# Optimization experiments

Measured on AMD Instinct MI355X. Metric: run time of the kernel, lower is better.

The kernel has to match this reference:

```python
import jax, jax.numpy as jnp
import numpy as np
from itertools import combinations

S = 7                       # number of species (H,C,N,O,S,F,Cl)
RCR, RCA = 5.2, 3.5         # radial / angular cutoffs (Angstrom)
ETA_R, ETA_A, ZETA = 19.7, 12.5, 14.1
SHF_R = jnp.asarray(0.8 + 0.275 * np.arange(16), jnp.float32)        # 16 radial shifts
SHF_A = jnp.asarray(0.8 + 0.3375 * np.arange(8), jnp.float32)        # 8 angular radial shifts
SHF_Z = jnp.asarray((np.arange(4) + 0.5) * np.pi / 4, jnp.float32)   # 4 angle shifts
NPAIR = S * (S + 1) // 2    # 28 unordered species pairs
_t = np.zeros((S, S), np.int32); _c = 0
for _a in range(S):
    for _b in range(_a, S):
        _t[_a, _b] = _t[_b, _a] = _c; _c += 1
TRIU = jnp.asarray(_t)
AEV_DIM = S * 16 + NPAIR * 32   # 1008
M, H1, H2, H3 = 8, 256, 192, 160  # ensemble size and MLP widths


def _fc(d, rc):
    # torchani cutoff_cosine, masked for safety beyond rc
    return jnp.where(d < rc, 0.5 * jnp.cos(jnp.pi * d / rc) + 0.5, 0.0)


def compute_aev(sp, coords, atom_index12, triplet_index):
    # sp:[N] int, coords:[N,3], atom_index12:[2,P] half neighbor list,
    # triplet_index:[3,T] = (center, neighbor_j, neighbor_k)
    N = sp.shape[0]
    i, j = atom_index12[0], atom_index12[1]
    dvec = coords[j] - coords[i]
    dist = jnp.sqrt((dvec * dvec).sum(-1))
    fc = _fc(dist, RCR)
    rterm = 0.25 * jnp.exp(-ETA_R * (dist[:, None] - SHF_R) ** 2) * fc[:, None]  # [P,16]
    rad = jnp.zeros((N * S, 16), rterm.dtype)
    rad = rad.at[i * S + sp[j]].add(rterm).at[j * S + sp[i]].add(rterm)
    rad = rad.reshape(N, S * 16)

    c, a, b = triplet_index[0], triplet_index[1], triplet_index[2]
    v1 = coords[a] - coords[c]
    v2 = coords[b] - coords[c]
    d1 = jnp.sqrt((v1 * v1).sum(-1))
    d2 = jnp.sqrt((v2 * v2).sum(-1))
    cosang = 0.95 * (v1 * v2).sum(-1) / (d1 * d2)   # 0.95 numerical-safety factor as in torchani
    ang = jnp.arccos(cosang)
    fcj = _fc(d1, RCA) * _fc(d2, RCA)
    f1 = ((1.0 + jnp.cos(ang[:, None] - SHF_Z)) / 2.0) ** ZETA              # [T,4]
    f2 = jnp.exp(-ETA_A * ((d1 + d2)[:, None] / 2.0 - SHF_A) ** 2)          # [T,8]
    aterm = 2.0 * (f2[:, :, None] * f1[:, None, :]).reshape(-1, 32) * fcj[:, None]  # [T,32]
    pidx = TRIU[sp[a], sp[b]]
    angv = jnp.zeros((N * NPAIR, 32), aterm.dtype).at[c * NPAIR + pidx].add(aterm)
    return jnp.concatenate([rad, angv.reshape(N, NPAIR * 32)], axis=-1)     # [N,1008]


def _energy_and_force(species, coordinates, atom_index12, triplet_index, sgp,
                      W1, b1, W2, b2, W3, b3, W4, b4, sae):
    sp = species[0]
    sgpv = sgp[0]

    def total(coords):
        aev = compute_aev(sp, coords[0], atom_index12, triplet_index)       # [N,1008]
        h = jax.nn.celu(jnp.einsum('na,msab->msnb', aev, W1) + b1[:, :, None, :], alpha=0.1)
        h = jax.nn.celu(jnp.einsum('msnb,msbc->msnc', h, W2) + b2[:, :, None, :], alpha=0.1)
        h = jax.nn.celu(jnp.einsum('msnc,mscd->msnd', h, W3) + b3[:, :, None, :], alpha=0.1)
        e = jnp.einsum('msnd,msd->msn', h, W4) + b4[:, :, None]             # [M,S,N]
        onehot = (sgpv[None, :] == jnp.arange(S)[:, None]).astype(e.dtype)  # ghosts (-1) -> all-zero
        atomic = (e * onehot[None]).sum(1).mean(0)                           # [N] ensemble mean
        atomic = atomic + jnp.where(sgpv >= 0, sae[jnp.clip(sgpv, 0)], 0.0)  # energy shifter SAEs
        return atomic.sum()

    E = total(coordinates)
    force = -jax.grad(total)(coordinates)   # autograd force as in forward_total
    return E[None], force


def setup_inputs() -> dict:
    key = jax.random.key(0)
    n = 14; N = n ** 3   # 2744 atoms on a jittered cubic lattice (2.5 A spacing)
    ar = np.arange(n)
    gx, gy, gz = np.meshgrid(ar, ar, ar, indexing='ij')
    pos = np.stack([gx, gy, gz], -1).reshape(-1, 3)
    lid = lambda p: (p[:, 0] * n + p[:, 1]) * n + p[:, 2]
    # half neighbor list: all lattice offsets with |r| <= 5.2/2.5 lattice units
    half = [(1,0,0),(0,1,0),(0,0,1),(1,1,0),(1,-1,0),(1,0,1),(1,0,-1),(0,1,1),(0,1,-1),
            (1,1,1),(1,1,-1),(1,-1,1),(1,-1,-1),(2,0,0),(0,2,0),(0,0,2)]
    ei, ej = [], []
    for off in half:
        q = pos + np.array(off)
        m = ((q >= 0) & (q < n)).all(1)
        ei.append(lid(pos[m])); ej.append(lid(q[m]))
    atom_index12 = np.stack([np.concatenate(ei), np.concatenate(ej)]).astype(np.int32)
    # angular triplets: pairs of unit-offset neighbors (within Rca=3.5 A) per center
    unit = [(1,0,0),(-1,0,0),(0,1,0),(0,-1,0),(0,0,1),(0,0,-1)]
    nb = np.full((N, 6), -1, np.int64)
    for t, off in enumerate(unit):
        q = pos + np.array(off)
        m = ((q >= 0) & (q < n)).all(1)
        nb[lid(pos[m]), t] = lid(q[m])
    tc, tj, tk = [], [], []
    for a_, b_ in combinations(range(6), 2):
        m = (nb[:, a_] >= 0) & (nb[:, b_] >= 0)
        tc.append(np.nonzero(m)[0]); tj.append(nb[m, a_]); tk.append(nb[m, b_])
    triplet_index = np.stack([np.concatenate(tc), np.concatenate(tj), np.concatenate(tk)]).astype(np.int32)
    rng = np.random.default_rng(0)
    species = rng.integers(0, S, (1, N)).astype(np.int32)
    nghost = 250
    sgp = species.copy(); sgp[0, N - nghost:] = -1   # ghost atoms padded with -1
    coords = (pos.astype(np.float32) * 2.5 + 0.15 * rng.standard_normal((N, 3)).astype(np.float32))[None]
    ks = jax.random.split(key, 9)
    D = AEV_DIM
    W1 = jax.random.normal(ks[0], (M, S, D, H1), jnp.float32) * (D ** -0.5)
    b1 = 0.01 * jax.random.normal(ks[1], (M, S, H1), jnp.float32)
    W2 = jax.random.normal(ks[2], (M, S, H1, H2), jnp.float32) * (H1 ** -0.5)
    b2 = 0.01 * jax.random.normal(ks[3], (M, S, H2), jnp.float32)
    W3 = jax.random.normal(ks[4], (M, S, H2, H3), jnp.float32) * (H2 ** -0.5)
    b3 = 0.01 * jax.random.normal(ks[5], (M, S, H3), jnp.float32)
    W4 = jax.random.normal(ks[6], (M, S, H3), jnp.float32) * (H3 ** -0.5)
    b4 = 0.01 * jax.random.normal(ks[7], (M, S), jnp.float32)
    sae = jax.random.normal(ks[8], (S,), jnp.float32)
    return {
        'species': jnp.asarray(species), 'coordinates': jnp.asarray(coords),
        'atom_index12': jnp.asarray(atom_index12), 'triplet_index': jnp.asarray(triplet_index),
        'species_ghost_as_padding': jnp.asarray(sgp),
        'W1': W1, 'b1': b1, 'W2': W2, 'b2': b2, 'W3': W3, 'b3': b3, 'W4': W4, 'b4': b4, 'sae': sae,
    }


def reference(species, coordinates, atom_index12, triplet_index, species_ghost_as_padding,
              W1, b1, W2, b2, W3, b3, W4, b4, sae):
    return _energy_and_force(species, coordinates, atom_index12, triplet_index,
                             species_ghost_as_padding, W1, b1, W2, b2, W3, b3, W4, b4, sae)
```

## Files before the change

kernel.cpp:

```cpp
#include <hip/hip_runtime.h>
#include <math.h>

constexpr int SPEC = 7;
constexpr int DAEV = 1008;
constexpr int RADN = 112;
constexpr int H1W = 256, H2W = 192, H3W = 160;
constexpr int MENS = 8;
constexpr float ALPHA = 0.1f;
constexpr float RCR_ = 5.2f, RCA_ = 3.5f;
constexpr float ETAR = 19.7f, ETAA = 12.5f, ZETA_ = 14.1f;
constexpr float PIF = 3.14159265358979323846f;

enum { MODE_FWD = 0, MODE_BWD = 1, MODE_PLAIN = 2 };

typedef _Float16 f16x8 __attribute__((ext_vector_type(8)));
typedef float f32x4 __attribute__((ext_vector_type(4)));

__device__ __forceinline__ f32x4 mfma16(f16x8 a, f16x8 b, f32x4 c) {
    return __builtin_amdgcn_mfma_f32_16x16x32_f16(a, b, c, 0, 0, 0);
}

__device__ __forceinline__ void cvt8(float4 u0, float4 u1, f16x8& h, f16x8& l) {
    float x[8] = {u0.x, u0.y, u0.z, u0.w, u1.x, u1.y, u1.z, u1.w};
    #pragma unroll
    for (int e = 0; e < 8; ++e) {
        _Float16 hh = (_Float16)x[e];
        h[e] = hh;
        l[e] = (_Float16)(x[e] - (float)hh);
    }
}

__global__ __launch_bounds__(256) void build_lists_k(
    const int* __restrict__ sgp, int* __restrict__ counts,
    int* __restrict__ lists, int N)
{
    int n = blockIdx.x * blockDim.x + threadIdx.x;
    if (n >= N) return;
    int g = sgp[n];
    if (g >= 0) {
        int p = atomicAdd(&counts[g], 1);
        lists[g * N + p] = n;
    }
}

__global__ __launch_bounds__(256) void radial_fwd_k(
    const int* __restrict__ ai12, const int* __restrict__ spec,
    const float* __restrict__ coord, float* __restrict__ aev, int P)
{
    int p = blockIdx.x * blockDim.x + threadIdx.x;
    if (p >= P) return;
    int i = ai12[p], j = ai12[P + p];
    float dx = coord[3 * j + 0] - coord[3 * i + 0];
    float dy = coord[3 * j + 1] - coord[3 * i + 1];
    float dz = coord[3 * j + 2] - coord[3 * i + 2];
    float d = sqrtf(dx * dx + dy * dy + dz * dz);
    float fc = (d < RCR_) ? (0.5f * cosf(PIF * d / RCR_) + 0.5f) : 0.f;
    int spi = spec[i], spj = spec[j];
    float* bi = aev + (size_t)i * DAEV + spj * 16;
    float* bj = aev + (size_t)j * DAEV + spi * 16;
    #pragma unroll
    for (int k = 0; k < 16; ++k) {
        float sh = 0.8f + 0.275f * k;
        float t = d - sh;
        float v = 0.25f * expf(-ETAR * t * t) * fc;
        atomicAdd(bi + k, v);
        atomicAdd(bj + k, v);
    }
}

__global__ __launch_bounds__(256) void angular_fwd_k(
    const int* __restrict__ tri, const int* __restrict__ spec,
    const float* __restrict__ coord, float* __restrict__ aev, int T)
{
    int t = blockIdx.x * blockDim.x + threadIdx.x;
    if (t >= T) return;
    int c = tri[t], a = tri[T + t], b = tri[2 * T + t];
    float cx = coord[3 * c], cy = coord[3 * c + 1], cz = coord[3 * c + 2];
    float v1x = coord[3 * a] - cx, v1y = coord[3 * a + 1] - cy, v1z = coord[3 * a + 2] - cz;
    float v2x = coord[3 * b] - cx, v2y = coord[3 * b + 1] - cy, v2z = coord[3 * b + 2] - cz;
    float d1 = sqrtf(v1x * v1x + v1y * v1y + v1z * v1z);
    float d2 = sqrtf(v2x * v2x + v2y * v2y + v2z * v2z);
    float u = v1x * v2x + v1y * v2y + v1z * v2z;
    float ca = 0.95f * u / (d1 * d2);
    float sa = sqrtf(fmaxf(1.f - ca * ca, 0.f));
    float fc1 = (d1 < RCA_) ? (0.5f * cosf(PIF * d1 / RCA_) + 0.5f) : 0.f;
    float fc2 = (d2 < RCA_) ? (0.5f * cosf(PIF * d2 / RCA_) + 0.5f) : 0.f;
    float fcj = fc1 * fc2;
    float savg = 0.5f * (d1 + d2);
    int s1 = spec[a], s2 = spec[b];
    int lo = min(s1, s2), hi = max(s1, s2);
    int pidx = lo * SPEC - (lo * (lo - 1)) / 2 + (hi - lo);
    float* ob = aev + (size_t)c * DAEV + RADN + pidx * 32;
    const float CZ[4] = {0.92387953f, 0.38268343f, -0.38268343f, -0.92387953f};
    const float SZ[4] = {0.38268343f, 0.92387953f, 0.92387953f, 0.38268343f};
    float f1[4];
    #pragma unroll
    for (int zz = 0; zz < 4; ++zz) {
        float cd = ca * CZ[zz] + sa * SZ[zz];
        float base = fmaxf(0.5f * (1.f + cd), 0.f);
        f1[zz] = powf(base, ZETA_);
    }
    #pragma unroll
    for (int q = 0; q < 8; ++q) {
        float sh = 0.8f + 0.3375f * q;
        float tq = savg - sh;
        float f2 = expf(-ETAA * tq * tq);
        float b2 = 2.f * f2 * fcj;
        #pragma unroll
        for (int zz = 0; zz < 4; ++zz)
            atomicAdd(ob + q * 4 + zz, b2 * f1[zz]);
    }
}

template<bool DO_O, bool DO_T>
__global__ __launch_bounds__(256) void wconv_k(
    const float* __restrict__ W,
    _Float16* __restrict__ oH, _Float16* __restrict__ oL,
    _Float16* __restrict__ tH, _Float16* __restrict__ tL,
    int K, int C, int ldt)
{
    __shared__ _Float16 sh[64][65];
    __shared__ _Float16 sl[64][65];
    const int z = blockIdx.z;
    const int k0 = blockIdx.y * 64, c0 = blockIdx.x * 64;
    const float* Wz = W + (size_t)z * K * C;
    const int c = threadIdx.x & 63, qr = threadIdx.x >> 6;
    #pragma unroll
    for (int rr = 0; rr < 16; ++rr) {
        int r = qr * 16 + rr;
        int k = k0 + r, cc = c0 + c;
        float v = (k < K && cc < C) ? Wz[(size_t)k * C + cc] : 0.f;
        _Float16 h = (_Float16)v;
        _Float16 l = (_Float16)(v - (float)h);
        if (DO_O && k < K && cc < C) {
            oH[(size_t)z * K * C + (size_t)k * C + cc] = h;
            oL[(size_t)z * K * C + (size_t)k * C + cc] = l;
        }
        if (DO_T) { sh[r][c] = h; sl[r][c] = l; }
    }
    if (DO_T) {
        __syncthreads();
        #pragma unroll
        for (int rr = 0; rr < 16; ++rr) {
            int r = qr * 16 + rr;
            int crow = c0 + r, kcol = k0 + c;
            if (crow < C && kcol < ldt) {
                tH[(size_t)z * C * ldt + (size_t)crow * ldt + kcol] = sh[c][r];
                tL[(size_t)z * C * ldt + (size_t)crow * ldt + kcol] = sl[c][r];
            }
        }
    }
}

template<int MODE, int ASRC, int BSRC, bool MCONCAT, int SPLITK>
__global__ __launch_bounds__(512) void mgemm_k(
    const void* __restrict__ Ah_, const void* __restrict__ Al_,
    const void* __restrict__ Bh_, const void* __restrict__ Bl_,
    const float* __restrict__ bias, float* __restrict__ cF,
    _Float16* __restrict__ cH, _Float16* __restrict__ cL,
    const int* __restrict__ lists, const int* __restrict__ counts,
    int N, int K, int KA, int H, int lda, int ldb, int ldc,
    size_t aStrM, size_t bStrZ, size_t cStrM)
{
    __shared__ f16x8 SM[3072];
    __shared__ int atomsS[64];
    #define AhS(g, kq, i) SM[(g) * 256 + (kq) * 64 + (i)]
    #define AlS(g, kq, i) SM[512 + (g) * 256 + (kq) * 64 + (i)]
    #define BhS(g, kq, c) SM[1024 + (g) * 512 + (kq) * 128 + (c)]
    #define BlS(g, kq, c) SM[2048 + (g) * 512 + (kq) * 128 + (c)]

    int bx = blockIdx.x, by = blockIdx.y, bz = blockIdx.z;
    if (gridDim.z == 56) {
        int BXY = gridDim.x * gridDim.y;
        int flat = bx + gridDim.x * (by + gridDim.y * bz);
        int xcd = flat & 7;
        int rest = flat >> 3;
        int zw = rest / BXY;
        int xy = rest - zw * BXY;
        bz = xcd * 7 + zw;
        bx = xy % gridDim.x;
        by = xy / gridDim.x;
    }

    const int z = bz;
    int m, sp_, chunk;
    if (MCONCAT) {
        sp_ = (SPLITK > 1) ? (z % SPEC) : z;
        chunk = (SPLITK > 1) ? (z / SPEC) : 0;
        m = 0;
    } else {
        m = z / SPEC; sp_ = z - m * SPEC; chunk = 0;
    }
    const int cnt = counts[sp_];
    const int row0 = by * 64;
    if (row0 >= cnt) return;
    const int col0 = bx * 128;
    const int tid = threadIdx.x;
    const int w = tid >> 6, lane = tid & 63;
    const int g = w >> 2, wl = w & 3;

    const int rA = min(row0 + lane, cnt - 1);
    const int atomA = lists[sp_ * N + rA];
    if (tid < 64) atomsS[tid] = atomA;

    const int bc0 = min(col0 + lane, H - 1);
    const int bc1 = min(col0 + 64 + lane, H - 1);

    f16x8 rAh, rAl;
    float4 rAf0, rAf1;
    f16x8 rBh0, rBl0, rBh1, rBl1;
    float4 rBq[4];
    float rB0f[8], rB1f[8];

    auto LOAD = [&](int k0s) {
        int kk = k0s + wl * 8;
        if constexpr (ASRC == 0) {
            const _Float16* ah = (const _Float16*)Ah_;
            const _Float16* al = (const _Float16*)Al_;
            size_t ao;
            if constexpr (MCONCAT) {
                int mm = kk >> 8, kr = kk & 255;
                ao = ((size_t)mm * N + atomA) * (size_t)lda + kr;
            } else {
                ao = (size_t)m * aStrM + (size_t)atomA * lda + kk;
            }
            rAh = *(const f16x8*)(ah + ao);
            rAl = *(const f16x8*)(al + ao);
        } else {
            const float* af = (const float*)Ah_;
            if (kk < KA) {
                const float* p = af + (size_t)atomA * lda + kk;
                rAf0 = *(const float4*)p;
                rAf1 = *(const float4*)(p + 4);
            } else {
                rAf0 = make_float4(0.f, 0.f, 0.f, 0.f);
                rAf1 = rAf0;
            }
        }
        if constexpr (BSRC == 0) {
            const _Float16* bh = (const _Float16*)Bh_;
            const _Float16* bl = (const _Float16*)Bl_;
            size_t b0 = (size_t)z * bStrZ + (size_t)bc0 * ldb + kk;
            size_t b1 = (size_t)z * bStrZ + (size_t)bc1 * ldb + kk;
            rBh0 = *(const f16x8*)(bh + b0);
            rBh1 = *(const f16x8*)(bh + b1);
            rBl0 = *(const f16x8*)(bl + b0);
            rBl1 = *(const f16x8*)(bl + b1);
        } else if constexpr (BSRC == 1) {
            const float* bf = (const float*)Bh_;
            int mm = kk >> 8, kr = kk & 255;
            size_t b0 = ((size_t)(mm * SPEC + sp_) * DAEV + bc0) * (size_t)ldb + kr;
            size_t b1 = ((size_t)(mm * SPEC + sp_) * DAEV + bc1) * (size_t)ldb + kr;
            rBq[0] = *(const float4*)(bf + b0);
            rBq[1] = *(const float4*)(bf + b0 + 4);
            rBq[2] = *(const float4*)(bf + b1);
            rBq[3] = *(const float4*)(bf + b1 + 4);
        } else {
            const float* bf = (const float*)Bh_ + (size_t)z * bStrZ;
            #pragma unroll
            for (int j = 0; j < 8; ++j) {
                int kg = kk + j;
                float v0 = 0.f, v1 = 0.f;
                if (kg < KA) {
                    v0 = bf[(size_t)kg * ldb + bc0];
                    v1 = bf[(size_t)kg * ldb + bc1];
                }
                rB0f[j] = v0;
                rB1f[j] = v1;
            }
        }
    };

    auto WRITE = [&]() {
        if constexpr (ASRC == 0) {
            AhS(g, wl, lane) = rAh;
            AlS(g, wl, lane) = rAl;
        } else {
            f16x8 h, l;
            cvt8(rAf0, rAf1, h, l);
            AhS(g, wl, lane) = h;
            AlS(g, wl, lane) = l;
        }
        if constexpr (BSRC == 0) {
            BhS(g, wl, lane) = rBh0;
            BhS(g, wl, 64 + lane) = rBh1;
            BlS(g, wl, lane) = rBl0;
            BlS(g, wl, 64 + lane) = rBl1;
        } else if constexpr (BSRC == 1) {
            f16x8 h, l;
            cvt8(rBq[0], rBq[1], h, l);
            BhS(g, wl, lane) = h;
            BlS(g, wl, lane) = l;
            cvt8(rBq[2], rBq[3], h, l);
            BhS(g, wl, 64 + lane) = h;
            BlS(g, wl, 64 + lane) = l;
        } else {
            f16x8 h0, l0, h1, l1;
            #pragma unroll
            for (int j = 0; j < 8; ++j) {
                _Float16 ha = (_Float16)rB0f[j];
                h0[j] = ha; l0[j] = (_Float16)(rB0f[j] - (float)ha);
                _Float16 hb = (_Float16)rB1f[j];
                h1[j] = hb; l1[j] = (_Float16)(rB1f[j] - (float)hb);
            }
            BhS(g, wl, lane) = h0;
            BlS(g, wl, lane) = l0;
            BhS(g, wl, 64 + lane) = h1;
            BlS(g, wl, 64 + lane) = l1;
        }
    };

    const int wr = wl >> 1, wc = wl & 1;
    const int fr = lane & 15, q = lane >> 4;

    f32x4 acc[2][4];
    #pragma unroll
    for (int mi = 0; mi < 2; ++mi)
        #pragma unroll
        for (int ni = 0; ni < 4; ++ni)
            acc[mi][ni] = (f32x4){0.f, 0.f, 0.f, 0.f};

    const int KC = (SPLITK > 1) ? (K / SPLITK) : K;
    const int kbeg = chunk * KC;
    const int ntT = KC / 32;
    const int nt0 = (ntT + 1) >> 1;
    const int my_nt = g ? (ntT - nt0) : nt0;
    const int gk = kbeg + (g ? nt0 * 32 : 0);

    if (my_nt > 0) LOAD(gk);

    for (int t = 0; t < nt0; ++t) {
        __syncthreads();
        if (t < my_nt) WRITE();
        __syncthreads();
        if (t + 1 < my_nt) LOAD(gk + (t + 1) * 32);

        if (t < my_nt) {
            f16x8 fah[2], fal[2], fbh[4], fbl[4];
            #pragma unroll
            for (int mi = 0; mi < 2; ++mi) {
                int r = wr * 32 + mi * 16 + fr;
                fah[mi] = AhS(g, q, r);
                fal[mi] = AlS(g, q, r);
            }
            #pragma unroll
            for (int ni = 0; ni < 4; ++ni) {
                int c = wc * 64 + ni * 16 + fr;
                fbh[ni] = BhS(g, q, c);
                fbl[ni] = BlS(g, q, c);
            }
            #pragma unroll
            for (int mi = 0; mi < 2; ++mi)
                #pragma unroll
                for (int ni = 0; ni < 4; ++ni) {
                    acc[mi][ni] = mfma16(fah[mi], fbl[ni], acc[mi][ni]);
                    acc[mi][ni] = mfma16(fal[mi], fbh[ni], acc[mi][ni]);
                    acc[mi][ni] = mfma16(fah[mi], fbh[ni], acc[mi][ni]);
                }
        }
    }

    __syncthreads();
    f32x4* X = (f32x4*)SM;
    const int xbase = (wl * 64 + lane) * 8;
    if (g == 1) {
        #pragma unroll
        for (int mi = 0; mi < 2; ++mi)
            #pragma unroll
            for (int ni = 0; ni < 4; ++ni)
                X[xbase + mi * 4 + ni] = acc[mi][ni];
    }
    __syncthreads();
    if (g == 1) return;
    #pragma unroll
    for (int mi = 0; mi < 2; ++mi)
        #pragma unroll
        for (int ni = 0; ni < 4; ++ni) {
            f32x4 o = X[xbase + mi * 4 + ni];
            acc[mi][ni] += o;
        }

    const float* brow = (MODE == MODE_FWD) ? (bias + (size_t)z * H) : nullptr;
    #pragma unroll
    for (int mi = 0; mi < 2; ++mi) {
        #pragma unroll
        for (int r = 0; r < 4; ++r) {
            int rl = wr * 32 + mi * 16 + q * 4 + r;
            if (row0 + rl >= cnt) continue;
            int atom = atomsS[rl];
            size_t rowoff = (size_t)m * cStrM + (size_t)atom * ldc;
            #pragma unroll
            for (int ni = 0; ni < 4; ++ni) {
                int col = col0 + wc * 64 + ni * 16 + fr;
                if (col >= H) continue;
                float v = acc[mi][ni][r];
                size_t idx = rowoff + col;
                if (MODE == MODE_FWD) {
                    v += brow[col];
                    v = (v > 0.f) ? v : ALPHA * expm1f(v * (1.f / ALPHA));
                    _Float16 hh = (_Float16)v;
                    cH[idx] = hh;
                    cL[idx] = (_Float16)(v - (float)hh);
                } else if (MODE == MODE_BWD) {
                    float hprev = (float)cH[idx] + (float)cL[idx];
                    float D = (hprev > 0.f) ? 1.f : (hprev * (1.f / ALPHA) + 1.f);
                    v *= D;
                    _Float16 hh = (_Float16)v;
                    cH[idx] = hh;
                    cL[idx] = (_Float16)(v - (float)hh);
                } else {
                    if (SPLITK > 1) atomicAdd(cF + idx, v);
                    else cF[idx] = v;
                }
            }
        }
    }
    #undef AhS
    #undef AlS
    #undef BhS
    #undef BlS
}

__global__ __launch_bounds__(256) void l4_k(
    _Float16* __restrict__ h3H, _Float16* __restrict__ h3L,
    const float* __restrict__ W4, const float* __restrict__ b4,
    const int* __restrict__ lists, const int* __restrict__ counts,
    float* __restrict__ Eout, int N)
{
    const int z = blockIdx.y;
    const int m = z / SPEC, s = z - m * SPEC;
    const int cnt = counts[s];
    const int sub = threadIdx.x >> 3;
    const int l8 = threadIdx.x & 7;
    const int row = blockIdx.x * 32 + sub;

    __shared__ float bsum;
    if (threadIdx.x == 0) bsum = 0.f;
    __syncthreads();

    if (row < cnt) {
        int atom = lists[s * N + row];
        size_t base = ((size_t)m * N + atom) * H3W;
        const float* w4 = W4 + (size_t)z * H3W;
        float sum = 0.f;
        for (int k = l8; k < H3W; k += 8) {
            float h = (float)h3H[base + k] + (float)h3L[base + k];
            float wv = w4[k];
            sum += h * wv;
            float D = (h > 0.f) ? 1.f : (h * 10.f + 1.f);
            float g = 0.125f * wv * D;
            _Float16 gh = (_Float16)g;
            h3H[base + k] = gh;
            h3L[base + k] = (_Float16)(g - (float)gh);
        }
        sum += __shfl_xor(sum, 1);
        sum += __shfl_xor(sum, 2);
        sum += __shfl_xor(sum, 4);
        if (l8 == 0) atomicAdd(&bsum, sum + b4[z]);
    }
    __syncthreads();
    if (threadIdx.x == 0) atomicAdd(Eout, 0.125f * bsum);
}

__global__ __launch_bounds__(256) void radial_bwd_k(
    const int* __restrict__ ai12, const int* __restrict__ spec,
    const float* __restrict__ coord, const float* __restrict__ daev,
    float* __restrict__ grad, int P)
{
    int p = blockIdx.x * blockDim.x + threadIdx.x;
    if (p >= P) return;
    int i = ai12[p], j = ai12[P + p];
    float dx = coord[3 * j + 0] - coord[3 * i + 0];
    float dy = coord[3 * j + 1] - coord[3 * i + 1];
    float dz = coord[3 * j + 2] - coord[3 * i + 2];
    float d = sqrtf(dx * dx + dy * dy + dz * dz);
    float fc, dfc;
    if (d < RCR_) {
        float ph = PIF * d / RCR_;
        fc = 0.5f * cosf(ph) + 0.5f;
        dfc = -0.5f * sinf(ph) * (PIF / RCR_);
    } else { fc = 0.f; dfc = 0.f; }
    int spi = spec[i], spj = spec[j];
    const float* gi = daev + (size_t)i * DAEV + spj * 16;
    const float* gj = daev + (size_t)j * DAEV + spi * 16;
    float gs = 0.f;
    #pragma unroll
    for (int k = 0; k < 16; ++k) {
        float sh = 0.8f + 0.275f * k;
        float t = d - sh;
        float ex = expf(-ETAR * t * t);
        float g = gi[k] + gj[k];
        gs += g * 0.25f * ex * (dfc - 2.f * ETAR * t * fc);
    }
    float invd = 1.f / d;
    float gx = gs * dx * invd, gy = gs * dy * invd, gz = gs * dz * invd;
    atomicAdd(&grad[3 * j + 0], gx);  atomicAdd(&grad[3 * j + 1], gy);  atomicAdd(&grad[3 * j + 2], gz);
    atomicAdd(&grad[3 * i + 0], -gx); atomicAdd(&grad[3 * i + 1], -gy); atomicAdd(&grad[3 * i + 2], -gz);
}

__global__ __launch_bounds__(256) void angular_bwd_k(
    const int* __restrict__ tri, const int* __restrict__ spec,
    const float* __restrict__ coord, const float* __restrict__ daev,
    float* __restrict__ grad, int T)
{
    int t = blockIdx.x * blockDim.x + threadIdx.x;
    if (t >= T) return;
    int c = tri[t], a = tri[T + t], b = tri[2 * T + t];
    float cx = coord[3 * c], cy = coord[3 * c + 1], cz = coord[3 * c + 2];
    float v1x = coord[3 * a] - cx, v1y = coord[3 * a + 1] - cy, v1z = coord[3 * a + 2] - cz;
    float v2x = coord[3 * b] - cx, v2y = coord[3 * b + 1] - cy, v2z = coord[3 * b + 2] - cz;
    float d1 = sqrtf(v1x * v1x + v1y * v1y + v1z * v1z);
    float d2 = sqrtf(v2x * v2x + v2y * v2y + v2z * v2z);
    float u = v1x * v2x + v1y * v2y + v1z * v2z;
    float inv12 = 1.f / (d1 * d2);
    float ca = 0.95f * u * inv12;
    float sa = sqrtf(fmaxf(1.f - ca * ca, 1e-12f));
    float fc1, dfc1, fc2, dfc2;
    if (d1 < RCA_) {
        float ph = PIF * d1 / RCA_;
        fc1 = 0.5f * cosf(ph) + 0.5f;
        dfc1 = -0.5f * sinf(ph) * (PIF / RCA_);
    } else { fc1 = 0.f; dfc1 = 0.f; }
    if (d2 < RCA_) {
        float ph = PIF * d2 / RCA_;
        fc2 = 0.5f * cosf(ph) + 0.5f;
        dfc2 = -0.5f * sinf(ph) * (PIF / RCA_);
    } else { fc2 = 0.f; dfc2 = 0.f; }
    float fcj = fc1 * fc2;
    float savg = 0.5f * (d1 + d2);
    int s1 = spec[a], s2 = spec[b];
    int lo = min(s1, s2), hi = max(s1, s2);
    int pidx = lo * SPEC - (lo * (lo - 1)) / 2 + (hi - lo);
    const float* gb = daev + (size_t)c * DAEV + RADN + pidx * 32;
    const float CZ[4] = {0.92387953f, 0.38268343f, -0.38268343f, -0.92387953f};
    const float SZ[4] = {0.38268343f, 0.92387953f, 0.92387953f, 0.38268343f};
    float f1[4], df1[4];
    #pragma unroll
    for (int zz = 0; zz < 4; ++zz) {
        float cd = ca * CZ[zz] + sa * SZ[zz];
        float sd = sa * CZ[zz] - ca * SZ[zz];
        float base = fmaxf(0.5f * (1.f + cd), 0.f);
        float pm1 = powf(base, ZETA_ - 1.f);
        f1[zz] = pm1 * base;
        df1[zz] = ZETA_ * pm1 * (-0.5f * sd);
    }
    float A_ = 0.f, B_ = 0.f, Cc = 0.f;
    #pragma unroll
    for (int q = 0; q < 8; ++q) {
        float sh = 0.8f + 0.3375f * q;
        float tq = savg - sh;
        float f2 = expf(-ETAA * tq * tq);
        float df2 = -ETAA * tq * f2;
        #pragma unroll
        for (int zz = 0; zz < 4; ++zz) {
            float G2 = 2.f * gb[q * 4 + zz];
            A_ += G2 * f2 * df1[zz];
            B_ += G2 * df2 * f1[zz];
            Cc += G2 * f2 * f1[zz];
        }
    }
    A_ *= fcj; B_ *= fcj;
    float C1 = Cc * dfc1 * fc2;
    float C2 = Cc * fc1 * dfc2;
    float cA = -A_ / sa;
    float k12 = cA * 0.95f * inv12;
    float coef1 = (cA * (-ca) / d1 + B_ + C1) / d1;
    float coef2 = (cA * (-ca) / d2 + B_ + C2) / d2;
    float g1x = coef1 * v1x + k12 * v2x;
    float g1y = coef1 * v1y + k12 * v2y;
    float g1z = coef1 * v1z + k12 * v2z;
    float g2x = coef2 * v2x + k12 * v1x;
    float g2y = coef2 * v2y + k12 * v1y;
    float g2z = coef2 * v2z + k12 * v1z;
    atomicAdd(&grad[3 * a + 0], g1x); atomicAdd(&grad[3 * a + 1], g1y); atomicAdd(&grad[3 * a + 2], g1z);
    atomicAdd(&grad[3 * b + 0], g2x); atomicAdd(&grad[3 * b + 1], g2y); atomicAdd(&grad[3 * b + 2], g2z);
    atomicAdd(&grad[3 * c + 0], -(g1x + g2x));
    atomicAdd(&grad[3 * c + 1], -(g1y + g2y));
    atomicAdd(&grad[3 * c + 2], -(g1z + g2z));
}

__global__ __launch_bounds__(256) void finalize_k(
    const float* __restrict__ grad, const int* __restrict__ sgp,
    const float* __restrict__ sae, float* __restrict__ out, int N)
{
    int n = blockIdx.x * blockDim.x + threadIdx.x;
    __shared__ float bs;
    if (threadIdx.x == 0) bs = 0.f;
    __syncthreads();
    float v = 0.f;
    if (n < N) {
        out[1 + 3 * n + 0] = -grad[3 * n + 0];
        out[1 + 3 * n + 1] = -grad[3 * n + 1];
        out[1 + 3 * n + 2] = -grad[3 * n + 2];
        int g = sgp[n];
        if (g >= 0) v = sae[g];
    }
    atomicAdd(&bs, v);
    __syncthreads();
    if (threadIdx.x == 0) atomicAdd(out, bs);
}

extern "C" void kernel_launch(void* const* d_in, const int* in_sizes, int n_in,
                              void* d_out, int out_size, void* d_ws, size_t ws_size,
                              hipStream_t stream)
{
    (void)n_in; (void)out_size; (void)ws_size;
    const int* species = (const int*)d_in[0];
    const float* coords = (const float*)d_in[1];
    const int* ai12 = (const int*)d_in[2];
    const int* tri = (const int*)d_in[3];
    const int* sgp = (const int*)d_in[4];
    const float* W1 = (const float*)d_in[5];
    const float* b1 = (const float*)d_in[6];
    const float* W2 = (const float*)d_in[7];
    const float* b2 = (const float*)d_in[8];
    const float* W3 = (const float*)d_in[9];
    const float* b3 = (const float*)d_in[10];
    const float* W4 = (const float*)d_in[11];
    const float* b4 = (const float*)d_in[12];
    const float* sae = (const float*)d_in[13];
    float* out = (float*)d_out;

    const int N = in_sizes[0];
    const int P = in_sizes[2] / 2;
    const int T = in_sizes[3] / 3;
    const size_t NM = (size_t)MENS * N;

    float* ws = (float*)d_ws;
    size_t off = 0;
    auto alloc = [&](size_t nf) { float* p = ws + off; off += nf; return p; };

    float* aev = alloc((size_t)N * DAEV);
    _Float16* H1h = (_Float16*)alloc(NM * 128);
    _Float16* H1l = (_Float16*)alloc(NM * 128);
    _Float16* H2h = (_Float16*)alloc(NM * 96);
    _Float16* H2l = (_Float16*)alloc(NM * 96);
    _Float16* H3h = (_Float16*)alloc(NM * 80);
    _Float16* H3l = (_Float16*)alloc(NM * 80);
    _Float16* Wh = (_Float16*)alloc((size_t)56 * 96 * 256);
    _Float16* Wl = (_Float16*)alloc((size_t)56 * 96 * 256);
    float* grad = alloc((size_t)N * 3);
    int* counts = (int*)alloc(8);
    int* lists = (int*)alloc((size_t)SPEC * N);
    float* daev = aev;

    hipMemsetAsync(aev, 0, (size_t)N * DAEV * sizeof(float), stream);
    hipMemsetAsync(grad, 0, (size_t)N * 3 * sizeof(float), stream);
    hipMemsetAsync(counts, 0, 8 * sizeof(int), stream);
    hipMemsetAsync(d_out, 0, sizeof(float), stream);

    build_lists_k<<<(N + 255) / 256, 256, 0, stream>>>(sgp, counts, lists, N);
    radial_fwd_k<<<(P + 255) / 256, 256, 0, stream>>>(ai12, species, coords, aev, P);
    angular_fwd_k<<<(T + 255) / 256, 256, 0, stream>>>(tri, species, coords, aev, T);

    const int rt = (N + 63) / 64;

    mgemm_k<MODE_FWD, 1, 2, false, 1><<<dim3(2, rt, 56), 512, 0, stream>>>(
        aev, nullptr, W1, nullptr, b1, nullptr, H1h, H1l,
        lists, counts, N, 1024, 1008, 256, 1008, 256, 256,
        0, (size_t)1008 * 256, (size_t)N * 256);

    wconv_k<false, true><<<dim3(3, 4, 56), 256, 0, stream>>>(
        W2, nullptr, nullptr, Wh, Wl, 256, 192, 256);
    mgemm_k<MODE_FWD, 0, 0, false, 1><<<dim3(2, rt, 56), 512, 0, stream>>>(
        H1h, H1l, Wh, Wl, b2, nullptr, H2h, H2l,
        lists, counts, N, 256, 256, 192, 256, 256, 192,
        (size_t)N * 256, (size_t)192 * 256, (size_t)N * 192);

    wconv_k<false, true><<<dim3(3, 3, 56), 256, 0, stream>>>(
        W3, nullptr, nullptr, Wh, Wl, 192, 160, 192);
    mgemm_k<MODE_FWD, 0, 0, false, 1><<<dim3(2, rt, 56), 512, 0, stream>>>(
        H2h, H2l, Wh, Wl, b3, nullptr, H3h, H3l,
        lists, counts, N, 192, 192, 160, 192, 192, 160,
        (size_t)N * 192, (size_t)160 * 192, (size_t)N * 160);

    l4_k<<<dim3((N + 31) / 32, 56), 256, 0, stream>>>(
        H3h, H3l, W4, b4, lists, counts, out, N);

    hipMemsetAsync(daev, 0, (size_t)N * DAEV * sizeof(float), stream);

    wconv_k<true, false><<<dim3(3, 3, 56), 256, 0, stream>>>(
        W3, Wh, Wl, nullptr, nullptr, 192, 160, 0);
    mgemm_k<MODE_BWD, 0, 0, false, 1><<<dim3(2, rt, 56), 512, 0, stream>>>(
        H3h, H3l, Wh, Wl, nullptr, nullptr, H2h, H2l,
        lists, counts, N, 160, 160, 192, 160, 160, 192,
        (size_t)N * 160, (size_t)192 * 160, (size_t)N * 192);

    wconv_k<true, false><<<dim3(3, 4, 56), 256, 0, stream>>>(
        W2, Wh, Wl, nullptr, nullptr, 256, 192, 0);
    mgemm_k<MODE_BWD, 0, 0, false, 1><<<dim3(2, rt, 56), 512, 0, stream>>>(
        H2h, H2l, Wh, Wl, nullptr, nullptr, H1h, H1l,
        lists, counts, N, 192, 192, 256, 192, 192, 256,
        (size_t)N * 192, (size_t)256 * 192, (size_t)N * 256);

    mgemm_k<MODE_PLAIN, 0, 1, true, 4><<<dim3(8, rt, 28), 512, 0, stream>>>(
        H1h, H1l, W1, nullptr, nullptr, daev, nullptr, nullptr,
        lists, counts, N, 2048, 2048, 1008, 256, 256, 1008,
        0, 0, 0);

    radial_bwd_k<<<(P + 255) / 256, 256, 0, stream>>>(ai12, species, coords, daev, grad, P);
    angular_bwd_k<<<(T + 255) / 256, 256, 0, stream>>>(tri, species, coords, daev, grad, T);
    finalize_k<<<(N + 255) / 256, 256, 0, stream>>>(grad, sgp, sae, out, N);
}
```

Before: 795.9 us.

## Compact per-species row tiles into a device-built plan to shrink GEMM grids

A tiny kernel builds a compacted list of (species, row-tile) entries from the per-species counts. The GEMM launches index that plan instead of launching a full rt-sized row grid for every species. This removes the many blocks that previously launched only to exit early because a species had few atoms. The XCD remapping now assigns the ensemble index by XCD, and the plan kernel adds one more serial launch.

```diff
diff --git a/kernel.cpp b/kernel.cpp
--- a/kernel.cpp
+++ b/kernel.cpp
@@ -40,6 +40,18 @@
     if (g >= 0) {
         int p = atomicAdd(&counts[g], 1);
         lists[g * N + p] = n;
+    }
+}
+
+__global__ void plan_k(const int* __restrict__ counts, int* __restrict__ plan)
+{
+    if (threadIdx.x == 0 && blockIdx.x == 0) {
+        int nt = 0;
+        for (int s = 0; s < SPEC; ++s) {
+            int k = (counts[s] + 63) >> 6;
+            for (int i = 0; i < k; ++i) plan[1 + nt++] = (s << 16) | i;
+        }
+        plan[0] = nt;
     }
 }
 
@@ -158,6 +170,7 @@
     const void* __restrict__ Bh_, const void* __restrict__ Bl_,
     const float* __restrict__ bias, float* __restrict__ cF,
     _Float16* __restrict__ cH, _Float16* __restrict__ cL,
+    const int* __restrict__ plan,
     const int* __restrict__ lists, const int* __restrict__ counts,
     int N, int K, int KA, int H, int lda, int ldb, int ldc,
     size_t aStrM, size_t bStrZ, size_t cStrM)
@@ -170,29 +183,24 @@
     #define BlS(g, kq, c) SM[2048 + (g) * 512 + (kq) * 128 + (c)]
 
     int bx = blockIdx.x, by = blockIdx.y, bz = blockIdx.z;
-    if (gridDim.z == 56) {
-        int BXY = gridDim.x * gridDim.y;
+    if (!MCONCAT && gridDim.z == 8) {
         int flat = bx + gridDim.x * (by + gridDim.y * bz);
-        int xcd = flat & 7;
+        bz = flat & 7;
         int rest = flat >> 3;
-        int zw = rest / BXY;
-        int xy = rest - zw * BXY;
-        bz = xcd * 7 + zw;
-        bx = xy % gridDim.x;
-        by = xy / gridDim.x;
-    }
-
-    const int z = bz;
-    int m, sp_, chunk;
-    if (MCONCAT) {
-        sp_ = (SPLITK > 1) ? (z % SPEC) : z;
-        chunk = (SPLITK > 1) ? (z / SPEC) : 0;
-        m = 0;
-    } else {
-        m = z / SPEC; sp_ = z - m * SPEC; chunk = 0;
-    }
+        bx = rest % gridDim.x;
+        by = rest / gridDim.x;
+    }
+
+    const int ntiles = plan[0];
+    if (by >= ntiles) return;
+    const int ent = plan[1 + by];
+    const int sp_ = ent >> 16;
+    const int row0 = (ent & 0xffff) << 6;
+    int m, chunk, zW;
+    if (MCONCAT) { m = 0; chunk = bz; zW = 0; }
+    else { m = bz; chunk = 0; zW = m * SPEC + sp_; }
+
     const int cnt = counts[sp_];
-    const int row0 = by * 64;
     if (row0 >= cnt) return;
     const int col0 = bx * 128;
     const int tid = threadIdx.x;
@@ -240,8 +248,8 @@
         if constexpr (BSRC == 0) {
             const _Float16* bh = (const _Float16*)Bh_;
             const _Float16* bl = (const _Float16*)Bl_;
-            size_t b0 = (size_t)z * bStrZ + (size_t)bc0 * ldb + kk;
-            size_t b1 = (size_t)z * bStrZ + (size_t)bc1 * ldb + kk;
+            size_t b0 = (size_t)zW * bStrZ + (size_t)bc0 * ldb + kk;
+            size_t b1 = (size_t)zW * bStrZ + (size_t)bc1 * ldb + kk;
             rBh0 = *(const f16x8*)(bh + b0);
             rBh1 = *(const f16x8*)(bh + b1);
             rBl0 = *(const f16x8*)(bl + b0);
@@ -256,7 +264,7 @@
             rBq[2] = *(const float4*)(bf + b1);
             rBq[3] = *(const float4*)(bf + b1 + 4);
         } else {
-            const float* bf = (const float*)Bh_ + (size_t)z * bStrZ;
+            const float* bf = (const float*)Bh_ + (size_t)zW * bStrZ;
             #pragma unroll
             for (int j = 0; j < 8; ++j) {
                 int kg = kk + j;
@@ -375,12 +383,10 @@
     #pragma unroll
     for (int mi = 0; mi < 2; ++mi)
         #pragma unroll
-        for (int ni = 0; ni < 4; ++ni) {
-            f32x4 o = X[xbase + mi * 4 + ni];
-            acc[mi][ni] += o;
-        }
-
-    const float* brow = (MODE == MODE_FWD) ? (bias + (size_t)z * H) : nullptr;
+        for (int ni = 0; ni < 4; ++ni)
+            acc[mi][ni] += X[xbase + mi * 4 + ni];
+
+    const float* brow = (MODE == MODE_FWD) ? (bias + (size_t)zW * H) : nullptr;
     #pragma unroll
     for (int mi = 0; mi < 2; ++mi) {
         #pragma unroll
@@ -641,6 +647,7 @@
     _Float16* Wl = (_Float16*)alloc((size_t)56 * 96 * 256);
     float* grad = alloc((size_t)N * 3);
     int* counts = (int*)alloc(8);
+    int* plan = (int*)alloc(64);
     int* lists = (int*)alloc((size_t)SPEC * N);
     float* daev = aev;
 
@@ -650,27 +657,28 @@
     hipMemsetAsync(d_out, 0, sizeof(float), stream);
 
     build_lists_k<<<(N + 255) / 256, 256, 0, stream>>>(sgp, counts, lists, N);
+    plan_k<<<1, 64, 0, stream>>>(counts, plan);
     radial_fwd_k<<<(P + 255) / 256, 256, 0, stream>>>(ai12, species, coords, aev, P);
     angular_fwd_k<<<(T + 255) / 256, 256, 0, stream>>>(tri, species, coords, aev, T);
 
-    const int rt = (N + 63) / 64;
-
-    mgemm_k<MODE_FWD, 1, 2, false, 1><<<dim3(2, rt, 56), 512, 0, stream>>>(
-        aev, nullptr, W1, nullptr, b1, nullptr, H1h, H1l,
+    const int YT = (N + 63) / 64 + SPEC;
+
+    mgemm_k<MODE_FWD, 1, 2, false, 1><<<dim3(2, YT, 8), 512, 0, stream>>>(
+        aev, nullptr, W1, nullptr, b1, nullptr, H1h, H1l, plan,
         lists, counts, N, 1024, 1008, 256, 1008, 256, 256,
         0, (size_t)1008 * 256, (size_t)N * 256);
 
     wconv_k<false, true><<<dim3(3, 4, 56), 256, 0, stream>>>(
         W2, nullptr, nullptr, Wh, Wl, 256, 192, 256);
-    mgemm_k<MODE_FWD, 0, 0, false, 1><<<dim3(2, rt, 56), 512, 0, stream>>>(
-        H1h, H1l, Wh, Wl, b2, nullptr, H2h, H2l,
+    mgemm_k<MODE_FWD, 0, 0, false, 1><<<dim3(2, YT, 8), 512, 0, stream>>>(
+        H1h, H1l, Wh, Wl, b2, nullptr, H2h, H2l, plan,
         lists, counts, N, 256, 256, 192, 256, 256, 192,
         (size_t)N * 256, (size_t)192 * 256, (size_t)N * 192);
 
     wconv_k<false, true><<<dim3(3, 3, 56), 256, 0, stream>>>(
         W3, nullptr, nullptr, Wh, Wl, 192, 160, 192);
-    mgemm_k<MODE_FWD, 0, 0, false, 1><<<dim3(2, rt, 56), 512, 0, stream>>>(
-        H2h, H2l, Wh, Wl, b3, nullptr, H3h, H3l,
+    mgemm_k<MODE_FWD, 0, 0, false, 1><<<dim3(2, YT, 8), 512, 0, stream>>>(
+        H2h, H2l, Wh, Wl, b3, nullptr, H3h, H3l, plan,
         lists, counts, N, 192, 192, 160, 192, 192, 160,
         (size_t)N * 192, (size_t)160 * 192, (size_t)N * 160);
 
@@ -681,20 +689,20 @@
 
     wconv_k<true, false><<<dim3(3, 3, 56), 256, 0, stream>>>(
         W3, Wh, Wl, nullptr, nullptr, 192, 160, 0);
-    mgemm_k<MODE_BWD, 0, 0, false, 1><<<dim3(2, rt, 56), 512, 0, stream>>>(
-        H3h, H3l, Wh, Wl, nullptr, nullptr, H2h, H2l,
+    mgemm_k<MODE_BWD, 0, 0, false, 1><<<dim3(2, YT, 8), 512, 0, stream>>>(
+        H3h, H3l, Wh, Wl, nullptr, nullptr, H2h, H2l, plan,
         lists, counts, N, 160, 160, 192, 160, 160, 192,
         (size_t)N * 160, (size_t)192 * 160, (size_t)N * 192);
 
     wconv_k<true, false><<<dim3(3, 4, 56), 256, 0, stream>>>(
         W2, Wh, Wl, nullptr, nullptr, 256, 192, 0);
-    mgemm_k<MODE_BWD, 0, 0, false, 1><<<dim3(2, rt, 56), 512, 0, stream>>>(
-        H2h, H2l, Wh, Wl, nullptr, nullptr, H1h, H1l,
+    mgemm_k<MODE_BWD, 0, 0, false, 1><<<dim3(2, YT, 8), 512, 0, stream>>>(
+        H2h, H2l, Wh, Wl, nullptr, nullptr, H1h, H1l, plan,
         lists, counts, N, 192, 192, 256, 192, 192, 256,
         (size_t)N * 192, (size_t)256 * 192, (size_t)N * 256);
 
-    mgemm_k<MODE_PLAIN, 0, 1, true, 4><<<dim3(8, rt, 28), 512, 0, stream>>>(
-        H1h, H1l, W1, nullptr, nullptr, daev, nullptr, nullptr,
+    mgemm_k<MODE_PLAIN, 0, 1, true, 4><<<dim3(8, YT, 4), 512, 0, stream>>>(
+        H1h, H1l, W1, nullptr, nullptr, daev, nullptr, nullptr, plan,
         lists, counts, N, 2048, 2048, 1008, 256, 256, 1008,
         0, 0, 0);
 
```

Measured after the change: 777.8 us. 2.3% less time.
